# Performance work log

Hardware: AMD Instinct MI355X
Metric: run time of the kernel (lower is better)

## Reference

```python
import jax, jax.numpy as jnp
import numpy as np

N = 50000        # nodes
E = 1600000      # edges (before self loops)
IN_DIM = 300     # input feature size
HID = 256        # hidden size
HEADS = 8
OC = HID // HEADS  # out channels per head = 32
LAYERS = 4
B = 1024         # number of target pairs
C = 3            # num classes
NEG_SLOPE = 0.2  # PyG GATConv leaky_relu slope


def setup_inputs() -> dict:
    key = jax.random.key(0)
    ks = jax.random.split(key, 12)

    def glorot(k, shape):
        lim = np.sqrt(6.0 / (shape[-2] + shape[-1]))
        return jax.random.uniform(k, shape, jnp.float32, -lim, lim)

    return {
        "x": jax.random.normal(ks[0], (N, IN_DIM), jnp.float32),
        "edge_index": jax.random.randint(ks[1], (2, E), 0, N, jnp.int64 if jax.config.jax_enable_x64 else jnp.int32),
        "target_mask": jax.random.randint(ks[2], (B, 2), 0, N, jnp.int64 if jax.config.jax_enable_x64 else jnp.int32),
        # lin1: [IN_DIM, HID] (stored pre-transposed vs torch)
        "lin1_W": glorot(ks[3], (IN_DIM, HID)),
        "lin1_b": jnp.zeros((HID,), jnp.float32),
        # stacked GATConv params
        "convs_W": glorot(ks[4], (LAYERS, HID, HEADS * OC)),
        "convs_att_dst": glorot(ks[5], (LAYERS, HEADS, OC)),  # att half applied to x_i (target)
        "convs_att_src": glorot(ks[6], (LAYERS, HEADS, OC)),  # att half applied to x_j (source)
        "convs_b": jnp.zeros((LAYERS, HID), jnp.float32),
        # lin3: [2*HID, C]
        "lin3_W": glorot(ks[7], (2 * HID, C)),
        "lin3_b": jnp.zeros((C,), jnp.float32),
    }


def gat_layer(h, src, tgt, W, att_dst, att_src, bias):
    """PyG-style GATConv (concat heads), edge list already includes self loops.
    h: [N, HID]; src/tgt: [E+N]; W: [HID, HEADS*OC]."""
    hw = (h @ W).reshape(N, HEADS, OC)
    # per-node attention scores, gathered per-edge (avoids materializing concat features)
    s_dst = jnp.einsum("nho,ho->nh", hw, att_dst)  # score for target role
    s_src = jnp.einsum("nho,ho->nh", hw, att_src)  # score for source role
    alpha = jax.nn.leaky_relu(s_dst[tgt] + s_src[src], NEG_SLOPE)  # [Etot, HEADS]
    # softmax over edges sharing the same target node (self loops => no empty segments)
    m = jax.ops.segment_max(alpha, tgt, num_segments=N)
    ex = jnp.exp(alpha - m[tgt])
    denom = jax.ops.segment_sum(ex, tgt, num_segments=N)
    a = ex / (denom[tgt] + 1e-16)
    # weighted scatter-aggregate of source features
    out = jax.ops.segment_sum(hw[src] * a[:, :, None], tgt, num_segments=N)  # [N, HEADS, OC]
    return out.reshape(N, HEADS * OC) + bias


def reference(x, edge_index, target_mask, lin1_W, lin1_b, convs_W,
              convs_att_dst, convs_att_src, convs_b, lin3_W, lin3_b):
    # add self loops once (PyG GATConv does this per layer; same edge set every layer)
    loop = jnp.arange(N, dtype=edge_index.dtype)
    src = jnp.concatenate([edge_index[0], loop])
    tgt = jnp.concatenate([edge_index[1], loop])

    h = x @ lin1_W + lin1_b
    for l in range(LAYERS):
        h = jax.nn.elu(gat_layer(h, src, tgt, convs_W[l],
                                 convs_att_dst[l], convs_att_src[l], convs_b[l]))
    # gather the two target nodes per sample and flatten -> [B, 2*HID]
    feats = h[target_mask].reshape(B, 2 * HID)
    logits = feats @ lin3_W + lin3_b
    return logits
```

## Files before the change

### kernel.cpp

```cpp
#include <hip/hip_runtime.h>
#include <math.h>

#define N_NODES 50000
#define N_PAD   50048
#define E_EDGES 1600000
#define ETOT    (E_EDGES + N_NODES)
#define EPAD    (E_EDGES + 8 * N_NODES)
#define IN_DIM  300
#define KP1     320
#define HID     256
#define HEADS   8
#define OC      32
#define LAYERS  4
#define BSAMP   1024
#define NEG_SLOPE 0.2f
#define DEG_CAP 128

#define NB     8
#define NPB    6250
#define BCAP   262144
#define NBLK_P 512
#define NBLK_S 196

typedef unsigned long long ull;
typedef _Float16 half8 __attribute__((ext_vector_type(8)));
typedef _Float16 half4v __attribute__((ext_vector_type(4)));
typedef float f32x4 __attribute__((ext_vector_type(4)));

#define GLDS16(g, l) __builtin_amdgcn_global_load_lds( \
    (const __attribute__((address_space(1))) void*)(g), \
    (__attribute__((address_space(3))) void*)(l), 16, 0, 0)


__global__ __launch_bounds__(256) void part_count_kernel(const int* __restrict__ tgt,
                                                         int* __restrict__ gcount) {
    __shared__ int cnt[NB];
    if (threadIdx.x < NB) cnt[threadIdx.x] = 0;
    __syncthreads();
    const int chunk = (ETOT + NBLK_P - 1) / NBLK_P;
    int beg = blockIdx.x * chunk;
    int end = min(beg + chunk, ETOT);
    for (int e = beg + threadIdx.x; e < end; e += 256) {
        int t_ = (e < E_EDGES) ? tgt[e] : (e - E_EDGES);
        atomicAdd(&cnt[t_ / NPB], 1);
    }
    __syncthreads();
    if (threadIdx.x < NB) gcount[blockIdx.x * NB + threadIdx.x] = cnt[threadIdx.x];
}

__global__ __launch_bounds__(512) void part_scan_kernel(const int* __restrict__ gcount,
                                                        int* __restrict__ goff,
                                                        int* __restrict__ bcnt) {
    __shared__ int arr[NBLK_P][NB];
    int k = threadIdx.x;
    int4 a = ((const int4*)gcount)[k * 2];
    int4 b = ((const int4*)gcount)[k * 2 + 1];
    int own[NB] = {a.x, a.y, a.z, a.w, b.x, b.y, b.z, b.w};
    #pragma unroll
    for (int j = 0; j < NB; j++) arr[k][j] = own[j];
    __syncthreads();
    for (int off = 1; off < NBLK_P; off <<= 1) {
        int tmp[NB];
        #pragma unroll
        for (int j = 0; j < NB; j++) tmp[j] = (k >= off) ? arr[k - off][j] : 0;
        __syncthreads();
        #pragma unroll
        for (int j = 0; j < NB; j++) arr[k][j] += tmp[j];
        __syncthreads();
    }
    int ex[NB];
    #pragma unroll
    for (int j = 0; j < NB; j++) ex[j] = arr[k][j] - own[j];
    ((int4*)goff)[k * 2]     = make_int4(ex[0], ex[1], ex[2], ex[3]);
    ((int4*)goff)[k * 2 + 1] = make_int4(ex[4], ex[5], ex[6], ex[7]);
    if (k == NBLK_P - 1) {
        #pragma unroll
        for (int j = 0; j < NB; j++) bcnt[j] = arr[k][j];
    }
}

__global__ __launch_bounds__(256) void part_scatter_kernel(const int* __restrict__ src,
                                                           const int* __restrict__ tgt,
                                                           const int* __restrict__ goff,
                                                           ull* __restrict__ bpart) {
    __shared__ int cur[NB];
    if (threadIdx.x < NB) cur[threadIdx.x] = goff[blockIdx.x * NB + threadIdx.x];
    __syncthreads();
    const int chunk = (ETOT + NBLK_P - 1) / NBLK_P;
    int beg = blockIdx.x * chunk;
    int end = min(beg + chunk, ETOT);
    for (int e = beg + threadIdx.x; e < end; e += 256) {
        int s_, t_;
        if (e < E_EDGES) { s_ = src[e]; t_ = tgt[e]; }
        else             { s_ = t_ = e - E_EDGES; }
        int b = t_ / NPB;
        int pos = atomicAdd(&cur[b], 1);
        bpart[(size_t)b * BCAP + pos] = ((ull)(unsigned)t_ << 32) | (unsigned)s_;
    }
}

__global__ __launch_bounds__(256) void count_edges_kernel(const ull* __restrict__ bpart,
                                                          const int* __restrict__ bcnt,
                                                          int* counts) {
    int b = blockIdx.x & (NB - 1);
    int ib = blockIdx.x >> 3;
    int nblk = gridDim.x >> 3;
    int nb = bcnt[b];
    const ull* bp = bpart + (size_t)b * BCAP;
    for (int i = ib * 256 + threadIdx.x; i < nb; i += nblk * 256)
        atomicAdd(&counts[(int)(bp[i] >> 32)], 1);
}

__global__ __launch_bounds__(256) void scan1_kernel(const int* __restrict__ counts,
                                                    int* __restrict__ row_ptr,
                                                    int* __restrict__ bsum) {
    __shared__ int sums[256];
    int t = threadIdx.x;
    int i = blockIdx.x * 256 + t;
    int c = (i < N_NODES) ? ((counts[i] + 7) & ~7) : 0;
    sums[t] = c;
    __syncthreads();
    for (int off = 1; off < 256; off <<= 1) {
        int a = sums[t];
        int u = (t >= off) ? sums[t - off] : 0;
        __syncthreads();
        sums[t] = a + u;
        __syncthreads();
    }
    if (i < N_NODES) row_ptr[i] = sums[t] - c;
    if (t == 255) bsum[blockIdx.x] = sums[255];
}

__global__ __launch_bounds__(256) void scan2_kernel(const int* __restrict__ bsum,
                                                    int* __restrict__ boff,
                                                    int* __restrict__ row_ptr) {
    __shared__ int sums[256];
    int t = threadIdx.x;
    int b = (t < NBLK_S) ? bsum[t] : 0;
    sums[t] = b;
    __syncthreads();
    for (int off = 1; off < 256; off <<= 1) {
        int a = sums[t];
        int u = (t >= off) ? sums[t - off] : 0;
        __syncthreads();
        sums[t] = a + u;
        __syncthreads();
    }
    if (t < NBLK_S) boff[t] = sums[t] - b;
    if (t == 255) row_ptr[N_NODES] = sums[255];
}

__global__ __launch_bounds__(256) void scan3_kernel(int* __restrict__ row_ptr,
                                                    const int* __restrict__ boff,
                                                    int* __restrict__ cursor) {
    int i = blockIdx.x * 256 + threadIdx.x;
    if (i >= N_NODES) return;
    int v = row_ptr[i] + boff[blockIdx.x];
    row_ptr[i] = v;
    cursor[i]  = v;
}

__global__ __launch_bounds__(256) void fill_edges_kernel(const ull* __restrict__ bpart,
                                                         const int* __restrict__ bcnt,
                                                         int* cursor, int* __restrict__ col) {
    int b = blockIdx.x & (NB - 1);
    int ib = blockIdx.x >> 3;
    int nblk = gridDim.x >> 3;
    int nb = bcnt[b];
    const ull* bp = bpart + (size_t)b * BCAP;
    for (int i = ib * 256 + threadIdx.x; i < nb; i += nblk * 256) {
        ull pk = bp[i];
        int t_ = (int)(pk >> 32);
        int s_ = (int)pk;
        int pos = atomicAdd(&cursor[t_], 1);
        col[pos] = s_;
    }
}

__global__ __launch_bounds__(256) void pad_edges_kernel(const int* __restrict__ cursor,
                                                        const int* __restrict__ row_ptr,
                                                        int* __restrict__ col) {
    int i = blockIdx.x * 256 + threadIdx.x;
    if (i >= N_NODES) return;
    int e = cursor[i];
    int pe = row_ptr[i + 1];
    for (; e < pe; e++) col[e] = i;
}


__global__ __launch_bounds__(256) void cast_x_kernel(const float* __restrict__ x, _Float16* __restrict__ xh) {
    int i = blockIdx.x * 256 + threadIdx.x;
    if (i >= N_NODES * (KP1 / 8)) return;
    int r = i / (KP1 / 8), c8 = i % (KP1 / 8);
    half8 o;
    const float4* xr = (const float4*)(x + (size_t)r * IN_DIM);
    if (c8 < 37) {
        float4 u = xr[c8 * 2], v = xr[c8 * 2 + 1];
        o[0] = (_Float16)u.x; o[1] = (_Float16)u.y; o[2] = (_Float16)u.z; o[3] = (_Float16)u.w;
        o[4] = (_Float16)v.x; o[5] = (_Float16)v.y; o[6] = (_Float16)v.z; o[7] = (_Float16)v.w;
    } else if (c8 == 37) {
        float4 u = xr[74];
        o[0] = (_Float16)u.x; o[1] = (_Float16)u.y; o[2] = (_Float16)u.z; o[3] = (_Float16)u.w;
        o[4] = o[5] = o[6] = o[7] = (_Float16)0.f;
    } else {
        #pragma unroll
        for (int j = 0; j < 8; j++) o[j] = (_Float16)0.f;
    }
    ((half8*)xh)[i] = o;
}

__global__ __launch_bounds__(256) void cast_w1_kernel(const float* __restrict__ W, _Float16* __restrict__ Wt) {
    int i = blockIdx.x * 256 + threadIdx.x;
    if (i >= HID * KP1) return;
    int n = i / KP1, k = i % KP1;
    float v = (k < IN_DIM) ? W[(size_t)k * HID + n] : 0.f;
    Wt[i] = (_Float16)v;
}

__global__ __launch_bounds__(256) void cast_wc_kernel(const float* __restrict__ W, _Float16* __restrict__ Wt) {
    int i = blockIdx.x * 256 + threadIdx.x;
    if (i >= LAYERS * HID * HID) return;
    int l = i / (HID * HID);
    int r = i % (HID * HID);
    int n = r / HID, k = r % HID;
    Wt[i] = (_Float16)W[(size_t)l * HID * HID + (size_t)k * HID + n];
}

__global__ __launch_bounds__(256) void gemm_mfma_kernel(const _Float16* __restrict__ A,
                                                        const _Float16* __restrict__ Wt,
                                                        const float* __restrict__ bias,
                                                        _Float16* __restrict__ C,
                                                        int M, int Kp, int addbias) {
    __shared__ _Float16 As[128][32];
    __shared__ _Float16 Bs[128][32];
    const int tid = threadIdx.x;
    const int m0 = blockIdx.x * 128;
    const int n0 = blockIdx.y * 128;
    const int w = tid >> 6, lane = tid & 63;
    const int wm = (w & 1) * 64, wn = (w >> 1) * 64;
    const int quad = lane >> 4, m16 = lane & 15;

    f32x4 acc[4][4];
    #pragma unroll
    for (int i = 0; i < 4; i++)
        #pragma unroll
        for (int j = 0; j < 4; j++)
            acc[i][j] = (f32x4){0.f, 0.f, 0.f, 0.f};

    char* lA = (char*)&As[0][0] + w * 1024;
    char* lB = (char*)&Bs[0][0] + w * 1024;

    for (int k0 = 0; k0 < Kp; k0 += 32) {
        #pragma unroll
        for (int i = 0; i < 2; i++) {
            int seg = tid + i * 256;
            int row = seg >> 2, off = seg & 3;
            GLDS16(&A[(size_t)(m0 + row) * Kp + k0 + off * 8], lA + i * 4096);
            GLDS16(&Wt[(size_t)(n0 + row) * Kp + k0 + off * 8], lB + i * 4096);
        }
        __syncthreads();

        half8 af[4], bf[4];
        #pragma unroll
        for (int i = 0; i < 4; i++) {
            af[i] = *(const half8*)&As[wm + i * 16 + m16][quad * 8];
            bf[i] = *(const half8*)&Bs[wn + i * 16 + m16][quad * 8];
        }
        #pragma unroll
        for (int mi = 0; mi < 4; mi++)
            #pragma unroll
            for (int ni = 0; ni < 4; ni++)
                acc[mi][ni] = __builtin_amdgcn_mfma_f32_16x16x32_f16(af[mi], bf[ni], acc[mi][ni], 0, 0, 0);
        __syncthreads();
    }

    #pragma unroll
    for (int mi = 0; mi < 4; mi++) {
        #pragma unroll
        for (int r = 0; r < 4; r++) {
            int row = m0 + wm + mi * 16 + quad * 4 + r;
            if (row < M) {
                #pragma unroll
                for (int ni = 0; ni < 4; ni++) {
                    int colg = n0 + wn + ni * 16 + m16;
                    float v = acc[mi][ni][r];
                    if (addbias) v += bias[colg];
                    C[(size_t)row * HID + colg] = (_Float16)v;
                }
            }
        }
    }
}

__global__ __launch_bounds__(256) void score_kernel(const _Float16* __restrict__ hw,
                                                    const float* __restrict__ att_dst,
                                                    const float* __restrict__ att_src,
                                                    float* __restrict__ s_dst,
                                                    float* __restrict__ s_src) {
    int wv = threadIdx.x >> 6, lane = threadIdx.x & 63;
    int nd = lane >> 3, hd = lane & 7;
    float4 ad[8], as4[8];
    const float4* A4d = (const float4*)att_dst;
    const float4* A4s = (const float4*)att_src;
    #pragma unroll
    for (int j = 0; j < 8; j++) { ad[j] = A4d[hd * 8 + j]; as4[j] = A4s[hd * 8 + j]; }
    const half8* hw8 = (const half8*)hw;
    int nwaves = gridDim.x * 4;
    for (int g = blockIdx.x * 4 + wv; g < N_NODES / 8; g += nwaves) {
        int node = g * 8 + nd;
        float sd = 0.f, ss = 0.f;
        #pragma unroll
        for (int k = 0; k < 4; k++) {
            half8 v = hw8[(size_t)node * 32 + hd * 4 + k];
            #pragma unroll
            for (int i = 0; i < 8; i++) {
                float f = (float)v[i];
                int q = k * 8 + i;
                sd += f * ((const float*)&ad[q >> 2])[q & 3];
                ss += f * ((const float*)&as4[q >> 2])[q & 3];
            }
        }
        s_dst[(size_t)g * 64 + lane] = sd;
        s_src[(size_t)g * 64 + lane] = ss;
    }
}

__global__ __launch_bounds__(256) void agg_kernel(const int* __restrict__ row_ptr,
                                                  const int* __restrict__ deg_arr,
                                                  const int* __restrict__ col,
                                                  const float* __restrict__ s_dst,
                                                  const float* __restrict__ s_src,
                                                  const _Float16* __restrict__ hw,
                                                  const float* __restrict__ bias,
                                                  _Float16* __restrict__ h_out) {
    __shared__ float exL[4][DEG_CAP * 8];
    __shared__ int  snL[4][DEG_CAP];

    int wv   = threadIdx.x >> 6;
    int lane = threadIdx.x & 63;
    int t = blockIdx.x * 4 + wv;
    if (t >= N_NODES) return;

    int start = row_ptr[t];
    int pdeg  = row_ptr[t + 1] - start;
    int deg   = deg_arr[t];

    int eh  = lane & 7;
    int ech = lane >> 3;
    float sd = s_dst[(size_t)t * HEADS + eh];

    if (pdeg <= DEG_CAP) {
        int ngrp = pdeg >> 3;
        float dsum = 0.f;
        for (int g = 0; g < ngrp; g++) {
            int slot = g * 8 + ech;
            int sn = col[start + slot];
            float a = sd + s_src[(size_t)sn * HEADS + eh];
            a = (a > 0.f) ? a : NEG_SLOPE * a;
            float exv = (slot < deg) ? __expf(a) : 0.f;
            exL[wv][slot * 8 + eh] = exv;
            if (eh == 0) snL[wv][slot] = sn;
            dsum += exv;
        }
        dsum += __shfl_xor(dsum, 8);
        dsum += __shfl_xor(dsum, 16);
        dsum += __shfl_xor(dsum, 32);

        int p  = lane >> 5;
        int c  = lane & 31;
        int hh = c >> 2;
        float inv = 1.f / (__shfl(dsum, hh) + 1e-16f);

        const half8* hw8 = (const half8*)hw;
        float acc[8] = {0.f, 0.f, 0.f, 0.f, 0.f, 0.f, 0.f, 0.f};

        for (int g = 0; g < ngrp; g++) {
            int base = g * 8;
            int   sns[4];
            half8 v[4];
            float ex[4];
            #pragma unroll
            for (int j = 0; j < 4; j++) sns[j] = snL[wv][base + 2 * j + p];
            #pragma unroll
            for (int j = 0; j < 4; j++) v[j] = hw8[(size_t)sns[j] * 32 + c];
            #pragma unroll
            for (int j = 0; j < 4; j++) ex[j] = exL[wv][(base + 2 * j + p) * 8 + hh];
            #pragma unroll
            for (int j = 0; j < 4; j++)
                #pragma unroll
                for (int i = 0; i < 8; i++)
                    acc[i] += ex[j] * (float)v[j][i];
        }

        #pragma unroll
        for (int i = 0; i < 8; i++) acc[i] += __shfl_xor(acc[i], 32);

        if (p == 0) {
            half8 ov;
            #pragma unroll
            for (int i = 0; i < 8; i++) {
                float o = acc[i] * inv + bias[c * 8 + i];
                o = (o > 0.f) ? o : (__expf(o) - 1.f);
                ov[i] = (_Float16)o;
            }
            ((half8*)h_out)[(size_t)t * 32 + c] = ov;
        }
    } else {
        int end = start + deg;
        float mx = -1e30f;
        for (int base = start; base < end; base += 8) {
            int e = base + ech;
            if (e < end) {
                int sn = col[e];
                float a = sd + s_src[(size_t)sn * HEADS + eh];
                a = (a > 0.f) ? a : NEG_SLOPE * a;
                mx = fmaxf(mx, a);
            }
        }
        mx = fmaxf(mx, __shfl_xor(mx, 8));
        mx = fmaxf(mx, __shfl_xor(mx, 16));
        mx = fmaxf(mx, __shfl_xor(mx, 32));

        float4 acc = {0.f, 0.f, 0.f, 0.f};
        float dsum = 0.f;
        const half4v* hw4 = (const half4v*)hw;
        int chead = lane >> 3;
        for (int base = start; base < end; base += 8) {
            int e = base + ech;
            float exv = 0.f;
            int sn = 0;
            if (e < end) {
                sn = col[e];
                float a = sd + s_src[(size_t)sn * HEADS + eh];
                a = (a > 0.f) ? a : NEG_SLOPE * a;
                exv = __expf(a - mx);
                dsum += exv;
            }
            int cnt = min(8, end - base);
            for (int j = 0; j < cnt; j++) {
                float exj = __shfl(exv, j * 8 + chead);
                int  snj  = __shfl(sn,  j * 8);
                half4v v = hw4[(size_t)snj * 64 + lane];
                acc.x += exj * (float)v[0];
                acc.y += exj * (float)v[1];
                acc.z += exj * (float)v[2];
                acc.w += exj * (float)v[3];
            }
        }
        dsum += __shfl_xor(dsum, 8);
        dsum += __shfl_xor(dsum, 16);
        dsum += __shfl_xor(dsum, 32);
        float den = __shfl(dsum, chead) + 1e-16f;
        float inv = 1.f / den;
        int cb = lane * 4;
        float o[4] = {acc.x * inv + bias[cb + 0], acc.y * inv + bias[cb + 1],
                      acc.z * inv + bias[cb + 2], acc.w * inv + bias[cb + 3]};
        #pragma unroll
        for (int i = 0; i < 4; i++) o[i] = (o[i] > 0.f) ? o[i] : (__expf(o[i]) - 1.f);
        half4v ov;
        ov[0] = (_Float16)o[0]; ov[1] = (_Float16)o[1];
        ov[2] = (_Float16)o[2]; ov[3] = (_Float16)o[3];
        ((half4v*)h_out)[(size_t)t * 64 + lane] = ov;
    }
}

__global__ __launch_bounds__(256) void head_kernel(const _Float16* __restrict__ h,
                                                   const int* __restrict__ target_mask,
                                                   const float* __restrict__ W,
                                                   const float* __restrict__ b,
                                                   float* __restrict__ out) {
    int s = blockIdx.x;
    int t = threadIdx.x;
    int n0 = target_mask[s * 2 + 0];
    int n1 = target_mask[s * 2 + 1];
    float f0 = (float)h[(size_t)n0 * HID + t];
    float f1 = (float)h[(size_t)n1 * HID + t];
    float a0 = f0 * W[t * 3 + 0] + f1 * W[(t + 256) * 3 + 0];
    float a1 = f0 * W[t * 3 + 1] + f1 * W[(t + 256) * 3 + 1];
    float a2 = f0 * W[t * 3 + 2] + f1 * W[(t + 256) * 3 + 2];
    #pragma unroll
    for (int off = 32; off >= 1; off >>= 1) {
        a0 += __shfl_xor(a0, off);
        a1 += __shfl_xor(a1, off);
        a2 += __shfl_xor(a2, off);
    }
    __shared__ float red[4][3];
    int wv = t >> 6, ln = t & 63;
    if (ln == 0) { red[wv][0] = a0; red[wv][1] = a1; red[wv][2] = a2; }
    __syncthreads();
    if (t < 3) {
        out[s * 3 + t] = red[0][t] + red[1][t] + red[2][t] + red[3][t] + b[t];
    }
}


extern "C" void kernel_launch(void* const* d_in, const int* in_sizes, int n_in,
                              void* d_out, int out_size, void* d_ws, size_t ws_size,
                              hipStream_t stream) {
    const float* x        = (const float*)d_in[0];
    const int*   eidx     = (const int*)  d_in[1];
    const int*   tmask    = (const int*)  d_in[2];
    const float* lin1_W   = (const float*)d_in[3];
    const float* lin1_b   = (const float*)d_in[4];
    const float* convs_W  = (const float*)d_in[5];
    const float* att_dst  = (const float*)d_in[6];
    const float* att_src  = (const float*)d_in[7];
    const float* convs_b  = (const float*)d_in[8];
    const float* lin3_W   = (const float*)d_in[9];
    const float* lin3_b   = (const float*)d_in[10];
    float* out = (float*)d_out;

    char* ws = (char*)d_ws;
    size_t off = 0;
    auto alloc = [&](size_t bytes) -> void* {
        void* p = ws + off;
        off = (off + bytes + 255) & ~(size_t)255;
        return p;
    };
    _Float16* xh   = (_Float16*)alloc((size_t)N_PAD * KP1 * 2);
    _Float16* h    = (_Float16*)alloc((size_t)N_PAD * HID * 2);
    _Float16* hw   = (_Float16*)alloc((size_t)N_NODES * HID * 2);
    _Float16* w1t  = (_Float16*)alloc((size_t)HID * KP1 * 2);
    _Float16* wct  = (_Float16*)alloc((size_t)LAYERS * HID * HID * 2);
    float* sdst    = (float*)alloc((size_t)N_NODES * HEADS * 4);
    float* ssrc    = (float*)alloc((size_t)N_NODES * HEADS * 4);
    int*   counts  = (int*)  alloc((size_t)N_NODES * 4);
    int*   rowptr  = (int*)  alloc((size_t)(N_NODES + 1) * 4);
    int*   cursor  = (int*)  alloc((size_t)N_NODES * 4);
    int*   col     = (int*)  alloc((size_t)EPAD * 4);
    ull*   bpart   = (ull*)  alloc((size_t)NB * BCAP * 8);
    int*   bcnt    = (int*)  alloc((size_t)NB * 4);
    int*   gcount  = (int*)  alloc((size_t)NBLK_P * NB * 4);
    int*   goff    = (int*)  alloc((size_t)NBLK_P * NB * 4);
    int*   bsum    = (int*)  alloc((size_t)NBLK_S * 4);
    int*   boff    = (int*)  alloc((size_t)NBLK_S * 4);

    const int* src = eidx;
    const int* tgt = eidx + E_EDGES;

    hipMemsetAsync(counts, 0, (size_t)N_NODES * 4, stream);
    part_count_kernel<<<NBLK_P, 256, 0, stream>>>(tgt, gcount);
    part_scan_kernel<<<1, NBLK_P, 0, stream>>>(gcount, goff, bcnt);
    part_scatter_kernel<<<NBLK_P, 256, 0, stream>>>(src, tgt, goff, bpart);
    count_edges_kernel<<<256, 256, 0, stream>>>(bpart, bcnt, counts);
    scan1_kernel<<<NBLK_S, 256, 0, stream>>>(counts, rowptr, bsum);
    scan2_kernel<<<1, 256, 0, stream>>>(bsum, boff, rowptr);
    scan3_kernel<<<NBLK_S, 256, 0, stream>>>(rowptr, boff, cursor);
    fill_edges_kernel<<<256, 256, 0, stream>>>(bpart, bcnt, cursor, col);
    pad_edges_kernel<<<(N_NODES + 255) / 256, 256, 0, stream>>>(cursor, rowptr, col);

    cast_x_kernel<<<(N_NODES * (KP1 / 8) + 255) / 256, 256, 0, stream>>>(x, xh);
    cast_w1_kernel<<<(HID * KP1 + 255) / 256, 256, 0, stream>>>(lin1_W, w1t);
    cast_wc_kernel<<<(LAYERS * HID * HID + 255) / 256, 256, 0, stream>>>(convs_W, wct);

    gemm_mfma_kernel<<<dim3((N_NODES + 127) / 128, HID / 128), 256, 0, stream>>>(
        xh, w1t, lin1_b, h, N_NODES, KP1, 1);

    for (int l = 0; l < LAYERS; l++) {
        gemm_mfma_kernel<<<dim3((N_NODES + 127) / 128, HID / 128), 256, 0, stream>>>(
            h, wct + (size_t)l * HID * HID, nullptr, hw, N_NODES, HID, 0);
        score_kernel<<<256, 256, 0, stream>>>(
            hw, att_dst + (size_t)l * HEADS * OC, att_src + (size_t)l * HEADS * OC, sdst, ssrc);
        agg_kernel<<<(N_NODES + 3) / 4, 256, 0, stream>>>(
            rowptr, counts, col, sdst, ssrc, hw, convs_b + (size_t)l * HID, h);
    }

    head_kernel<<<BSAMP, 256, 0, stream>>>(h, tmask, lin3_W, lin3_b, out);
}
```

Measured before the change: 945.9 us.

## Split GAT aggregation into two half-head passes over 4 heads each

Splits the per-node aggregation kernel into two launches, each handling 4 of the 8 heads (128 of 256 channels). Each wave processes 16 edge slots per step instead of 8, so more distinct source rows are gathered in parallel and the hw working set per pass is halved, aiming for better cache hit rates on the random gathers. The cost is an extra launch per layer, re-reading col/s_src twice, and the high-degree fallback path runs only in the first pass. Padded slots beyond pdeg now use the node itself as a dummy source with zero weight.

After: 952.4 us. No clear change (+0.7%).

```diff
diff --git a/kernel.cpp b/kernel.cpp
--- a/kernel.cpp
+++ b/kernel.cpp
@@ -332,8 +332,9 @@
                                                   const float* __restrict__ s_src,
                                                   const _Float16* __restrict__ hw,
                                                   const float* __restrict__ bias,
-                                                  _Float16* __restrict__ h_out) {
-    __shared__ float exL[4][DEG_CAP * 8];
+                                                  _Float16* __restrict__ h_out,
+                                                  int hbase) {
+    __shared__ float exL[4][DEG_CAP * 4];
     __shared__ int  snL[4][DEG_CAP];
 
     int wv   = threadIdx.x >> 6;
@@ -345,67 +346,72 @@
     int pdeg  = row_ptr[t + 1] - start;
     int deg   = deg_arr[t];
 
-    int eh  = lane & 7;
-    int ech = lane >> 3;
-    float sd = s_dst[(size_t)t * HEADS + eh];
-
     if (pdeg <= DEG_CAP) {
-        int ngrp = pdeg >> 3;
+        int sl = lane >> 2;
+        int eh = lane & 3;
+        float sd = s_dst[(size_t)t * HEADS + hbase + eh];
+        int pdeg16 = (pdeg + 15) & ~15;
         float dsum = 0.f;
-        for (int g = 0; g < ngrp; g++) {
-            int slot = g * 8 + ech;
-            int sn = col[start + slot];
-            float a = sd + s_src[(size_t)sn * HEADS + eh];
+        for (int s0 = 0; s0 < pdeg16; s0 += 16) {
+            int slot = s0 + sl;
+            int sn = (slot < pdeg) ? col[start + slot] : t;
+            float a = sd + s_src[(size_t)sn * HEADS + hbase + eh];
             a = (a > 0.f) ? a : NEG_SLOPE * a;
             float exv = (slot < deg) ? __expf(a) : 0.f;
-            exL[wv][slot * 8 + eh] = exv;
+            exL[wv][slot * 4 + eh] = exv;
             if (eh == 0) snL[wv][slot] = sn;
             dsum += exv;
         }
+        dsum += __shfl_xor(dsum, 4);
         dsum += __shfl_xor(dsum, 8);
         dsum += __shfl_xor(dsum, 16);
         dsum += __shfl_xor(dsum, 32);
 
-        int p  = lane >> 5;
-        int c  = lane & 31;
+        int c = lane & 15, j = lane >> 4;
         int hh = c >> 2;
         float inv = 1.f / (__shfl(dsum, hh) + 1e-16f);
 
         const half8* hw8 = (const half8*)hw;
         float acc[8] = {0.f, 0.f, 0.f, 0.f, 0.f, 0.f, 0.f, 0.f};
 
-        for (int g = 0; g < ngrp; g++) {
-            int base = g * 8;
+        for (int s0 = 0; s0 < pdeg16; s0 += 16) {
             int   sns[4];
             half8 v[4];
             float ex[4];
             #pragma unroll
-            for (int j = 0; j < 4; j++) sns[j] = snL[wv][base + 2 * j + p];
-            #pragma unroll
-            for (int j = 0; j < 4; j++) v[j] = hw8[(size_t)sns[j] * 32 + c];
-            #pragma unroll
-            for (int j = 0; j < 4; j++) ex[j] = exL[wv][(base + 2 * j + p) * 8 + hh];
-            #pragma unroll
-            for (int j = 0; j < 4; j++)
+            for (int u = 0; u < 4; u++) sns[u] = snL[wv][s0 + u * 4 + j];
+            #pragma unroll
+            for (int u = 0; u < 4; u++) v[u] = hw8[(size_t)sns[u] * 32 + hbase * 4 + c];
+            #pragma unroll
+            for (int u = 0; u < 4; u++) ex[u] = exL[wv][(s0 + u * 4 + j) * 4 + hh];
+            #pragma unroll
+            for (int u = 0; u < 4; u++)
                 #pragma unroll
                 for (int i = 0; i < 8; i++)
-                    acc[i] += ex[j] * (float)v[j][i];
-        }
-
-        #pragma unroll
-        for (int i = 0; i < 8; i++) acc[i] += __shfl_xor(acc[i], 32);
-
-        if (p == 0) {
+                    acc[i] += ex[u] * (float)v[u][i];
+        }
+
+        #pragma unroll
+        for (int i = 0; i < 8; i++) {
+            acc[i] += __shfl_xor(acc[i], 16);
+            acc[i] += __shfl_xor(acc[i], 32);
+        }
+
+        if (j == 0) {
             half8 ov;
             #pragma unroll
             for (int i = 0; i < 8; i++) {
-                float o = acc[i] * inv + bias[c * 8 + i];
+                float o = acc[i] * inv + bias[hbase * 32 + c * 8 + i];
                 o = (o > 0.f) ? o : (__expf(o) - 1.f);
                 ov[i] = (_Float16)o;
             }
-            ((half8*)h_out)[(size_t)t * 32 + c] = ov;
+            ((half8*)h_out)[(size_t)t * 32 + hbase * 4 + c] = ov;
         }
     } else {
+        if (hbase != 0) return;
+        int eh  = lane & 7;
+        int ech = lane >> 3;
+        float sd = s_dst[(size_t)t * HEADS + eh];
         int end = start + deg;
         float mx = -1e30f;
         for (int base = start; base < end; base += 8) {
@@ -437,9 +443,9 @@
                 dsum += exv;
             }
             int cnt = min(8, end - base);
-            for (int j = 0; j < cnt; j++) {
-                float exj = __shfl(exv, j * 8 + chead);
-                int  snj  = __shfl(sn,  j * 8);
+            for (int j2 = 0; j2 < cnt; j2++) {
+                float exj = __shfl(exv, j2 * 8 + chead);
+                int  snj  = __shfl(sn,  j2 * 8);
                 half4v v = hw4[(size_t)snj * 64 + lane];
                 acc.x += exj * (float)v[0];
                 acc.y += exj * (float)v[1];
@@ -562,7 +568,9 @@
         score_kernel<<<256, 256, 0, stream>>>(
             hw, att_dst + (size_t)l * HEADS * OC, att_src + (size_t)l * HEADS * OC, sdst, ssrc);
         agg_kernel<<<(N_NODES + 3) / 4, 256, 0, stream>>>(
-            rowptr, counts, col, sdst, ssrc, hw, convs_b + (size_t)l * HID, h);
+            rowptr, counts, col, sdst, ssrc, hw, convs_b + (size_t)l * HID, h, 0);
+        agg_kernel<<<(N_NODES + 3) / 4, 256, 0, stream>>>(
+            rowptr, counts, col, sdst, ssrc, hw, convs_b + (size_t)l * HID, h, 4);
     }
 
     head_kernel<<<BSAMP, 256, 0, stream>>>(h, tmask, lin3_W, lin3_b, out);
```
